# Performance work log

Measured on AMD Instinct MI355X. Metric: run time of the kernel, lower is better.

Reference implementation:

```python
import jax, jax.numpy as jnp
import numpy as np

N, L, S, D, K, H, G = 512, 1024, 3, 128, 4, 32, 64


def setup_inputs() -> dict:
    key = jax.random.key(0)
    ks = jax.random.split(key, 12)
    f = lambda i, shape, s=1.0: jax.random.normal(ks[i], shape, dtype=jnp.float32) * s
    return dict(
        scores=f(0, (N, 1, L, S)),
        veh_repr=f(1, (N, 1, D)),
        cust_repr=f(2, (N, L, D)),
        edge_emb=f(3, (N, 1, L, D)),
        expert_w1=f(4, (K, S, H), 0.3),
        expert_b1=jnp.zeros((K, H), jnp.float32),
        expert_w2=f(5, (K, H, 1), 0.3),
        expert_b2=jnp.zeros((K, 1), jnp.float32),
        sit_w1=f(6, (2 * D, G), 0.05),
        sit_b1=jnp.zeros((G,), jnp.float32),
        sit_w2=f(7, (G, K), 0.1),
        sit_b2=jnp.zeros((K,), jnp.float32),
        cand_w=f(8, (S, K), 0.3),
        cand_b=jnp.zeros((K,), jnp.float32),
        edge_w=f(9, (D, K), 0.05),
        gate_balance=jnp.zeros((), jnp.float32),
    )


def reference(scores, veh_repr, cust_repr, edge_emb,
              expert_w1, expert_b1, expert_w2, expert_b2,
              sit_w1, sit_b1, sit_w2, sit_b2,
              cand_w, cand_b, edge_w, gate_balance):
    # Inference mode: no gate noise, no dropout (identity at eval).
    # Situation gating: vehicle repr + graph context -> (N,1,K) logits
    graph_ctx = cust_repr.mean(axis=1, keepdims=True)              # (N,1,D)
    sit_in = jnp.concatenate([veh_repr, graph_ctx], axis=-1)       # (N,1,2D)
    hg = jax.nn.gelu(sit_in @ sit_w1 + sit_b1, approximate=False)  # (N,1,G)
    sit_logits = hg @ sit_w2 + sit_b2                              # (N,1,K)

    # Candidate-level gating from raw scores + edge embeddings
    cand_logits = scores @ cand_w + cand_b + edge_emb @ edge_w     # (N,1,L,K)

    alpha = jax.nn.sigmoid(gate_balance)
    gate_logits = alpha * sit_logits[:, :, None, :] + (1.0 - alpha) * cand_logits
    gate_w = jax.nn.softmax(gate_logits, axis=-1)                  # (N,1,L,K)

    # Per-expert tiny MLP over the S score channels
    h = jax.nn.gelu(jnp.einsum('nqls,ksh->nqlkh', scores, expert_w1) + expert_b1,
                    approximate=False)                             # (N,1,L,K,H)
    expert_out = jnp.einsum('nqlkh,kho->nqlko', h, expert_w2)[..., 0] + expert_b2[:, 0]

    fused = (gate_w * expert_out).sum(axis=-1)                     # (N,1,L)
    return fused
```

## Files before the change

### kernel.cpp

```cpp
#include <hip/hip_runtime.h>

#define NN 512
#define LL 1024
#define SS 3
#define DD 128
#define KK 4
#define HH 32
#define GG 64

#define DPP_XOR1 0xB1
#define DPP_XOR2 0x4E
#define DPP_ROR4 0x124
#define DPP_ROR8 0x128
#define SWZ16 0x401F

template <int CTRL>
__device__ __forceinline__ float dppf(float x) {
    return __int_as_float(__builtin_amdgcn_update_dpp(
        0, __float_as_int(x), CTRL, 0xF, 0xF, true));
}
__device__ __forceinline__ float swz16f(float x) {
    return __int_as_float(__builtin_amdgcn_ds_swizzle(__float_as_int(x), SWZ16));
}

__device__ __forceinline__ float fast_gelu(float x) {
    const float c0 = 0.7978845608028654f;
    const float c1 = 0.7978845608028654f * 0.044715f;
    float u = x * x;
    float y = x * fmaf(c1, u, c0);
    float e = __expf(2.0f * y);
    float r = __builtin_amdgcn_rcpf(e + 1.0f);
    float t = fmaf(-2.0f, r, 1.0f);
    return 0.5f * x * (1.0f + t);
}

__global__ __launch_bounds__(512, 4) void k_all(
    const float* __restrict__ scores, const float* __restrict__ veh,
    const float* __restrict__ cust, const float* __restrict__ edge,
    const float* __restrict__ ew1, const float* __restrict__ eb1,
    const float* __restrict__ ew2, const float* __restrict__ eb2,
    const float* __restrict__ sw1, const float* __restrict__ sb1,
    const float* __restrict__ sw2, const float* __restrict__ sb2,
    const float* __restrict__ cand_w, const float* __restrict__ cand_b,
    const float* __restrict__ edge_w, const float* __restrict__ gbp,
    float* __restrict__ out)
{
    __shared__ float4 red[512];
    __shared__ float sin_[2 * DD];
    __shared__ float hg[GG];
    __shared__ float slds[KK];
    __shared__ float4 sc4[(LL * SS) / 4];
    __shared__ float elds[LL * 8];

    const int n = blockIdx.x;
    const int t = threadIdx.x;
    const int lane = t & 63;
    const int r = lane & 31;

    const int ko = r & 3;
    const int jg = r >> 2;
    const bool kb0 = (r & 1) != 0;
    const bool kb1 = (r & 2) != 0;

    {
        const float4* sp4 = (const float4*)(scores + (size_t)n * LL * SS);
        sc4[t] = sp4[t];
        if (t < 256) sc4[512 + t] = sp4[512 + t];
    }

    const float4* ew4 = (const float4*)edge_w;
    const float4 wqa = ew4[4 * r + 0];
    const float4 wqb = ew4[4 * r + 1];
    const float4 wqc = ew4[4 * r + 2];
    const float4 wqd = ew4[4 * r + 3];
    const float cw0 = cand_w[0 * KK + ko];
    const float cw1 = cand_w[1 * KK + ko];
    const float cw2 = cand_w[2 * KK + ko];
    const float cb  = cand_b[ko];
    const float4* w1f = (const float4*)ew1;
    const float4 w1a = w1f[(ko * SS + 0) * (HH / 4) + jg];
    const float4 w1b = w1f[(ko * SS + 1) * (HH / 4) + jg];
    const float4 w1c = w1f[(ko * SS + 2) * (HH / 4) + jg];
    const float4 b1v = ((const float4*)eb1)[ko * (HH / 4) + jg];
    const float4 w2v = ((const float4*)ew2)[ko * (HH / 4) + jg];
    const float b2o8 = 0.125f * eb2[ko];
    const float gbv = gbp[0];
    const float alpha = 1.0f / (1.0f + __expf(-gbv));
    const float onema = 1.0f - alpha;
    const float cbase = onema * cb;

    __syncthreads();

    const int c = t & 31;
    const int rs = t >> 5;
    const float4* cp = (const float4*)(cust + (size_t)n * LL * DD);
    const int base_el = t >> 5;
    const float* sc_lds = (const float*)sc4;
    const float* ed_base = edge + (size_t)n * LL * DD;

    float4 a0 = make_float4(0.f, 0.f, 0.f, 0.f), a1 = a0, a2 = a0, a3 = a0;

    for (int i = 0; i < 16; ++i) {
        const int e0 = base_el + i * 64;

        float4 ev[4];
        #pragma unroll
        for (int u = 0; u < 4; ++u)
            ev[u] = *(const float4*)(ed_base + (size_t)(e0 + u * 16) * DD + r * 4);
        float4 v0 = cp[(rs + 16 * i      ) * 32 + c];
        float4 v1 = cp[(rs + 16 * i + 256) * 32 + c];
        float4 v2 = cp[(rs + 16 * i + 512) * 32 + c];
        float4 v3 = cp[(rs + 16 * i + 768) * 32 + c];

        float s0[4], s1[4], s2[4];
        #pragma unroll
        for (int u = 0; u < 4; ++u) {
            const int el = e0 + u * 16;
            s0[u] = sc_lds[el * 3 + 0];
            s1[u] = sc_lds[el * 3 + 1];
            s2[u] = sc_lds[el * 3 + 2];
        }

        float p0[4], p1[4], p2[4], p3[4];
        #pragma unroll
        for (int u = 0; u < 4; ++u) {
            p0[u] = fmaf(ev[u].x, wqa.x, fmaf(ev[u].y, wqb.x, fmaf(ev[u].z, wqc.x, ev[u].w * wqd.x)));
            p1[u] = fmaf(ev[u].x, wqa.y, fmaf(ev[u].y, wqb.y, fmaf(ev[u].z, wqc.y, ev[u].w * wqd.y)));
            p2[u] = fmaf(ev[u].x, wqa.z, fmaf(ev[u].y, wqb.z, fmaf(ev[u].z, wqc.z, ev[u].w * wqd.z)));
            p3[u] = fmaf(ev[u].x, wqa.w, fmaf(ev[u].y, wqb.w, fmaf(ev[u].z, wqc.w, ev[u].w * wqd.w)));
        }
        float P0[4], P2[4];
        #pragma unroll
        for (int u = 0; u < 4; ++u) {
            float g0 = kb0 ? p0[u] : p1[u];
            float g2 = kb0 ? p2[u] : p3[u];
            float k0 = kb0 ? p1[u] : p0[u];
            float k2 = kb0 ? p3[u] : p2[u];
            P0[u] = k0 + dppf<DPP_XOR1>(g0);
            P2[u] = k2 + dppf<DPP_XOR1>(g2);
        }
        float q[4];
        #pragma unroll
        for (int u = 0; u < 4; ++u) {
            float gv = kb1 ? P0[u] : P2[u];
            float kv = kb1 ? P2[u] : P0[u];
            q[u] = kv + dppf<DPP_XOR2>(gv);
        }
        #pragma unroll
        for (int u = 0; u < 4; ++u) q[u] += dppf<DPP_ROR4>(q[u]);
        #pragma unroll
        for (int u = 0; u < 4; ++u) q[u] += dppf<DPP_ROR8>(q[u]);
        #pragma unroll
        for (int u = 0; u < 4; ++u) q[u] += swz16f(q[u]);

        float exc[4];
        #pragma unroll
        for (int u = 0; u < 4; ++u) {
            float sdot = fmaf(s0[u], cw0, fmaf(s1[u], cw1, s2[u] * cw2));
            exc[u] = __expf(fmaf(onema, sdot + q[u], cbase));
        }

        float vq[4];
        #pragma unroll
        for (int u = 0; u < 4; ++u) {
            float z, h, acc;
            z = fmaf(s0[u], w1a.x, fmaf(s1[u], w1b.x, fmaf(s2[u], w1c.x, b1v.x))); h = fast_gelu(z); acc = h * w2v.x;
            z = fmaf(s0[u], w1a.y, fmaf(s1[u], w1b.y, fmaf(s2[u], w1c.y, b1v.y))); h = fast_gelu(z); acc = fmaf(h, w2v.y, acc);
            z = fmaf(s0[u], w1a.z, fmaf(s1[u], w1b.z, fmaf(s2[u], w1c.z, b1v.z))); h = fast_gelu(z); acc = fmaf(h, w2v.z, acc);
            z = fmaf(s0[u], w1a.w, fmaf(s1[u], w1b.w, fmaf(s2[u], w1c.w, b1v.w))); h = fast_gelu(z); acc = fmaf(h, w2v.w, acc);
            vq[u] = exc[u] * (acc + b2o8);
        }
        #pragma unroll
        for (int u = 0; u < 4; ++u) vq[u] += dppf<DPP_ROR4>(vq[u]);
        #pragma unroll
        for (int u = 0; u < 4; ++u) vq[u] += dppf<DPP_ROR8>(vq[u]);
        #pragma unroll
        for (int u = 0; u < 4; ++u) vq[u] += swz16f(vq[u]);

        if (r < 8) {
            #pragma unroll
            for (int u = 0; u < 4; ++u) {
                const int el = e0 + u * 16;
                elds[el * 8 + r] = (r < 4) ? vq[u] : exc[u];
            }
        }

        a0.x += v0.x; a0.y += v0.y; a0.z += v0.z; a0.w += v0.w;
        a1.x += v1.x; a1.y += v1.y; a1.z += v1.z; a1.w += v1.w;
        a2.x += v2.x; a2.y += v2.y; a2.z += v2.z; a2.w += v2.w;
        a3.x += v3.x; a3.y += v3.y; a3.z += v3.z; a3.w += v3.w;
    }

    a0.x += a1.x + a2.x + a3.x;
    a0.y += a1.y + a2.y + a3.y;
    a0.z += a1.z + a2.z + a3.z;
    a0.w += a1.w + a2.w + a3.w;
    red[t] = a0;
    __syncthreads();

    if (t < 32) {
        float4 s = red[t];
        #pragma unroll
        for (int i = 1; i < 16; i++) {
            float4 v = red[i * 32 + t];
            s.x += v.x; s.y += v.y; s.z += v.z; s.w += v.w;
        }
        const float inv = 1.0f / (float)LL;
        sin_[DD + 4 * t + 0] = s.x * inv;
        sin_[DD + 4 * t + 1] = s.y * inv;
        sin_[DD + 4 * t + 2] = s.z * inv;
        sin_[DD + 4 * t + 3] = s.w * inv;
        float4 vv = ((const float4*)(veh + (size_t)n * DD))[t];
        sin_[4 * t + 0] = vv.x; sin_[4 * t + 1] = vv.y;
        sin_[4 * t + 2] = vv.z; sin_[4 * t + 3] = vv.w;
    }
    __syncthreads();

    float* redf = (float*)red;
    if (t < 256) {
        const int g = t & 63;
        const int part = t >> 6;
        float a = 0.f;
        #pragma unroll 8
        for (int i = 0; i < 64; ++i) {
            const int row = part * 64 + i;
            a = fmaf(sin_[row], sw1[row * GG + g], a);
        }
        redf[t] = a;
    }
    __syncthreads();
    if (t < GG) {
        float a = sb1[t] + redf[t] + redf[t + 64] + redf[t + 128] + redf[t + 192];
        hg[t] = fast_gelu(a);
    }
    __syncthreads();
    if (t < KK) {
        float a = sb2[t];
        #pragma unroll
        for (int g = 0; g < GG; g++)
            a = fmaf(hg[g], sw2[g * KK + t], a);
        slds[t] = a;
    }
    __syncthreads();

    const float m0 = __expf(alpha * slds[0]);
    const float m1 = __expf(alpha * slds[1]);
    const float m2 = __expf(alpha * slds[2]);
    const float m3 = __expf(alpha * slds[3]);
    float* out_base = out + (size_t)n * LL;
    #pragma unroll
    for (int e = t; e < LL; e += 512) {
        const float4 V = *(const float4*)&elds[e * 8];
        const float4 E = *(const float4*)&elds[e * 8 + 4];
        float num = fmaf(m0, V.x, fmaf(m1, V.y, fmaf(m2, V.z, m3 * V.w)));
        float den = fmaf(m0, E.x, fmaf(m1, E.y, fmaf(m2, E.z, m3 * E.w)));
        out_base[e] = num * __builtin_amdgcn_rcpf(den);
    }
}

extern "C" void kernel_launch(void* const* d_in, const int* in_sizes, int n_in,
                              void* d_out, int out_size, void* d_ws, size_t ws_size,
                              hipStream_t stream)
{
    const float* scores = (const float*)d_in[0];
    const float* veh    = (const float*)d_in[1];
    const float* cust   = (const float*)d_in[2];
    const float* edge   = (const float*)d_in[3];
    const float* ew1    = (const float*)d_in[4];
    const float* eb1    = (const float*)d_in[5];
    const float* ew2    = (const float*)d_in[6];
    const float* eb2    = (const float*)d_in[7];
    const float* sw1    = (const float*)d_in[8];
    const float* sb1    = (const float*)d_in[9];
    const float* sw2    = (const float*)d_in[10];
    const float* sb2    = (const float*)d_in[11];
    const float* cw     = (const float*)d_in[12];
    const float* cb     = (const float*)d_in[13];
    const float* egw    = (const float*)d_in[14];
    const float* gb     = (const float*)d_in[15];
    float* out = (float*)d_out;

    hipLaunchKernelGGL(k_all, dim3(NN), dim3(512), 0, stream,
                       scores, veh, cust, edge, ew1, eb1, ew2, eb2,
                       sw1, sb1, sw2, sb2, cw, cb, egw, gb, out);
}
```

Baseline: 537.5 us.

## Software-pipeline edge embedding loads and alias score/reduction shared buffers

```diff
diff --git a/kernel.cpp b/kernel.cpp
--- a/kernel.cpp
+++ b/kernel.cpp
@@ -33,6 +33,94 @@
     float t = fmaf(-2.0f, r, 1.0f);
     return 0.5f * x * (1.0f + t);
 }
+
+#define BODY(I, EVC, EVN, PF)                                                   \
+  {                                                                             \
+    const int e0 = base_el + (I) * 64;                                          \
+                         \
+    float4 v0 = cp[(base_el + 16 * (I)      ) * 32 + r];                        \
+    float4 v1 = cp[(base_el + 16 * (I) + 256) * 32 + r];                        \
+    float4 v2 = cp[(base_el + 16 * (I) + 512) * 32 + r];                        \
+    float4 v3 = cp[(base_el + 16 * (I) + 768) * 32 + r];                        \
+    if (PF) {                                                                   \
+      _Pragma("unroll")                                                         \
+      for (int u = 0; u < 4; ++u)                                               \
+        EVN[u] = *(const float4*)(ed_base + (size_t)(e0 + 64 + u * 16) * DD + r * 4); \
+    }                                                                           \
+    float s0[4], s1[4], s2[4];                                                  \
+    _Pragma("unroll")                                                           \
+    for (int u = 0; u < 4; ++u) {                                               \
+      const int el = e0 + u * 16;                                               \
+      s0[u] = sc_lds[el * 3 + 0];                                               \
+      s1[u] = sc_lds[el * 3 + 1];                                               \
+      s2[u] = sc_lds[el * 3 + 2];                                               \
+    }                                                                           \
+    float p0[4], p1[4], p2[4], p3[4];                                           \
+    _Pragma("unroll")                                                           \
+    for (int u = 0; u < 4; ++u) {                                               \
+      p0[u] = fmaf(EVC[u].x, wqa.x, fmaf(EVC[u].y, wqb.x, fmaf(EVC[u].z, wqc.x, EVC[u].w * wqd.x))); \
+      p1[u] = fmaf(EVC[u].x, wqa.y, fmaf(EVC[u].y, wqb.y, fmaf(EVC[u].z, wqc.y, EVC[u].w * wqd.y))); \
+      p2[u] = fmaf(EVC[u].x, wqa.z, fmaf(EVC[u].y, wqb.z, fmaf(EVC[u].z, wqc.z, EVC[u].w * wqd.z))); \
+      p3[u] = fmaf(EVC[u].x, wqa.w, fmaf(EVC[u].y, wqb.w, fmaf(EVC[u].z, wqc.w, EVC[u].w * wqd.w))); \
+    }                                                                           \
+    float P0[4], P2[4];                                                         \
+    _Pragma("unroll")                                                           \
+    for (int u = 0; u < 4; ++u) {                                               \
+      float g0 = kb0 ? p0[u] : p1[u];                                           \
+      float g2 = kb0 ? p2[u] : p3[u];                                           \
+      float k0 = kb0 ? p1[u] : p0[u];                                           \
+      float k2 = kb0 ? p3[u] : p2[u];                                           \
+      P0[u] = k0 + dppf<DPP_XOR1>(g0);                                          \
+      P2[u] = k2 + dppf<DPP_XOR1>(g2);                                          \
+    }                                                                           \
+    float q[4];                                                                 \
+    _Pragma("unroll")                                                           \
+    for (int u = 0; u < 4; ++u) {                                               \
+      float gv = kb1 ? P0[u] : P2[u];                                           \
+      float kv = kb1 ? P2[u] : P0[u];                                           \
+      q[u] = kv + dppf<DPP_XOR2>(gv);                                           \
+    }                                                                           \
+    _Pragma("unroll")                                                           \
+    for (int u = 0; u < 4; ++u) q[u] += dppf<DPP_ROR4>(q[u]);                   \
+    _Pragma("unroll")                                                           \
+    for (int u = 0; u < 4; ++u) q[u] += dppf<DPP_ROR8>(q[u]);                   \
+    _Pragma("unroll")                                                           \
+    for (int u = 0; u < 4; ++u) q[u] += swz16f(q[u]);                           \
+    float exc[4];                                                               \
+    _Pragma("unroll")                                                           \
+    for (int u = 0; u < 4; ++u) {                                               \
+      float sdot = fmaf(s0[u], cw0, fmaf(s1[u], cw1, s2[u] * cw2));             \
+      exc[u] = __expf(fmaf(onema, sdot + q[u], cbase));                         \
+    }                                                                           \
+    float vq[4];                                                                \
+    _Pragma("unroll")                                                           \
+    for (int u = 0; u < 4; ++u) {                                               \
+      float z, h, acc;                                                          \
+      z = fmaf(s0[u], w1a.x, fmaf(s1[u], w1b.x, fmaf(s2[u], w1c.x, b1v.x))); h = fast_gelu(z); acc = h * w2v.x; \
+      z = fmaf(s0[u], w1a.y, fmaf(s1[u], w1b.y, fmaf(s2[u], w1c.y, b1v.y))); h = fast_gelu(z); acc = fmaf(h, w2v.y, acc); \
+      z = fmaf(s0[u], w1a.z, fmaf(s1[u], w1b.z, fmaf(s2[u], w1c.z, b1v.z))); h = fast_gelu(z); acc = fmaf(h, w2v.z, acc); \
+      z = fmaf(s0[u], w1a.w, fmaf(s1[u], w1b.w, fmaf(s2[u], w1c.w, b1v.w))); h = fast_gelu(z); acc = fmaf(h, w2v.w, acc); \
+      vq[u] = exc[u] * (acc + b2o8);                                            \
+    }                                                                           \
+    _Pragma("unroll")                                                           \
+    for (int u = 0; u < 4; ++u) vq[u] += dppf<DPP_ROR4>(vq[u]);                 \
+    _Pragma("unroll")                                                           \
+    for (int u = 0; u < 4; ++u) vq[u] += dppf<DPP_ROR8>(vq[u]);                 \
+    _Pragma("unroll")                                                           \
+    for (int u = 0; u < 4; ++u) vq[u] += swz16f(vq[u]);                         \
+    if (r < 8) {                                                                \
+      _Pragma("unroll")                                                         \
+      for (int u = 0; u < 4; ++u) {                                             \
+        const int el = e0 + u * 16;                                             \
+        elds[el * 8 + r] = (r < 4) ? vq[u] : exc[u];                            \
+      }                                                                         \
+    }                                                                           \
+             \
+    a0.x += (v0.x + v1.x) + (v2.x + v3.x);                                      \
+    a0.y += (v0.y + v1.y) + (v2.y + v3.y);                                      \
+    a0.z += (v0.z + v1.z) + (v2.z + v3.z);                                      \
+    a0.w += (v0.w + v1.w) + (v2.w + v3.w);                                      \
+  }
 
 __global__ __launch_bounds__(512, 4) void k_all(
     const float* __restrict__ scores, const float* __restrict__ veh,
@@ -45,17 +133,16 @@
     const float* __restrict__ edge_w, const float* __restrict__ gbp,
     float* __restrict__ out)
 {
-    __shared__ float4 red[512];
+    __shared__ float shbuf[3072];
     __shared__ float sin_[2 * DD];
     __shared__ float hg[GG];
     __shared__ float slds[KK];
-    __shared__ float4 sc4[(LL * SS) / 4];
     __shared__ float elds[LL * 8];
 
     const int n = blockIdx.x;
     const int t = threadIdx.x;
-    const int lane = t & 63;
-    const int r = lane & 31;
+    const int r = t & 31;
+    const int base_el = t >> 5;
 
     const int ko = r & 3;
     const int jg = r >> 2;
@@ -64,6 +151,7 @@
 
     {
         const float4* sp4 = (const float4*)(scores + (size_t)n * LL * SS);
+        float4* sc4 = (float4*)shbuf;
         sc4[t] = sp4[t];
         if (t < 256) sc4[512 + t] = sp4[512 + t];
     }
@@ -76,7 +164,6 @@
     const float cw0 = cand_w[0 * KK + ko];
     const float cw1 = cand_w[1 * KK + ko];
     const float cw2 = cand_w[2 * KK + ko];
-    const float cb  = cand_b[ko];
     const float4* w1f = (const float4*)ew1;
     const float4 w1a = w1f[(ko * SS + 0) * (HH / 4) + jg];
     const float4 w1b = w1f[(ko * SS + 1) * (HH / 4) + jg];
@@ -84,125 +171,40 @@
     const float4 b1v = ((const float4*)eb1)[ko * (HH / 4) + jg];
     const float4 w2v = ((const float4*)ew2)[ko * (HH / 4) + jg];
     const float b2o8 = 0.125f * eb2[ko];
-    const float gbv = gbp[0];
-    const float alpha = 1.0f / (1.0f + __expf(-gbv));
+    const float alpha = 1.0f / (1.0f + __expf(-gbp[0]));
     const float onema = 1.0f - alpha;
-    const float cbase = onema * cb;
-
-    __syncthreads();
-
-    const int c = t & 31;
-    const int rs = t >> 5;
+    const float cbase = onema * cand_b[ko];
+
+    __syncthreads();
+
+    const float* sc_lds = shbuf;
     const float4* cp = (const float4*)(cust + (size_t)n * LL * DD);
-    const int base_el = t >> 5;
-    const float* sc_lds = (const float*)sc4;
     const float* ed_base = edge + (size_t)n * LL * DD;
 
-    float4 a0 = make_float4(0.f, 0.f, 0.f, 0.f), a1 = a0, a2 = a0, a3 = a0;
-
-    for (int i = 0; i < 16; ++i) {
-        const int e0 = base_el + i * 64;
-
-        float4 ev[4];
-        #pragma unroll
-        for (int u = 0; u < 4; ++u)
-            ev[u] = *(const float4*)(ed_base + (size_t)(e0 + u * 16) * DD + r * 4);
-        float4 v0 = cp[(rs + 16 * i      ) * 32 + c];
-        float4 v1 = cp[(rs + 16 * i + 256) * 32 + c];
-        float4 v2 = cp[(rs + 16 * i + 512) * 32 + c];
-        float4 v3 = cp[(rs + 16 * i + 768) * 32 + c];
-
-        float s0[4], s1[4], s2[4];
-        #pragma unroll
-        for (int u = 0; u < 4; ++u) {
-            const int el = e0 + u * 16;
-            s0[u] = sc_lds[el * 3 + 0];
-            s1[u] = sc_lds[el * 3 + 1];
-            s2[u] = sc_lds[el * 3 + 2];
-        }
-
-        float p0[4], p1[4], p2[4], p3[4];
-        #pragma unroll
-        for (int u = 0; u < 4; ++u) {
-            p0[u] = fmaf(ev[u].x, wqa.x, fmaf(ev[u].y, wqb.x, fmaf(ev[u].z, wqc.x, ev[u].w * wqd.x)));
-            p1[u] = fmaf(ev[u].x, wqa.y, fmaf(ev[u].y, wqb.y, fmaf(ev[u].z, wqc.y, ev[u].w * wqd.y)));
-            p2[u] = fmaf(ev[u].x, wqa.z, fmaf(ev[u].y, wqb.z, fmaf(ev[u].z, wqc.z, ev[u].w * wqd.z)));
-            p3[u] = fmaf(ev[u].x, wqa.w, fmaf(ev[u].y, wqb.w, fmaf(ev[u].z, wqc.w, ev[u].w * wqd.w)));
-        }
-        float P0[4], P2[4];
-        #pragma unroll
-        for (int u = 0; u < 4; ++u) {
-            float g0 = kb0 ? p0[u] : p1[u];
-            float g2 = kb0 ? p2[u] : p3[u];
-            float k0 = kb0 ? p1[u] : p0[u];
-            float k2 = kb0 ? p3[u] : p2[u];
-            P0[u] = k0 + dppf<DPP_XOR1>(g0);
-            P2[u] = k2 + dppf<DPP_XOR1>(g2);
-        }
-        float q[4];
-        #pragma unroll
-        for (int u = 0; u < 4; ++u) {
-            float gv = kb1 ? P0[u] : P2[u];
-            float kv = kb1 ? P2[u] : P0[u];
-            q[u] = kv + dppf<DPP_XOR2>(gv);
-        }
-        #pragma unroll
-        for (int u = 0; u < 4; ++u) q[u] += dppf<DPP_ROR4>(q[u]);
-        #pragma unroll
-        for (int u = 0; u < 4; ++u) q[u] += dppf<DPP_ROR8>(q[u]);
-        #pragma unroll
-        for (int u = 0; u < 4; ++u) q[u] += swz16f(q[u]);
-
-        float exc[4];
-        #pragma unroll
-        for (int u = 0; u < 4; ++u) {
-            float sdot = fmaf(s0[u], cw0, fmaf(s1[u], cw1, s2[u] * cw2));
-            exc[u] = __expf(fmaf(onema, sdot + q[u], cbase));
-        }
-
-        float vq[4];
-        #pragma unroll
-        for (int u = 0; u < 4; ++u) {
-            float z, h, acc;
-            z = fmaf(s0[u], w1a.x, fmaf(s1[u], w1b.x, fmaf(s2[u], w1c.x, b1v.x))); h = fast_gelu(z); acc = h * w2v.x;
-            z = fmaf(s0[u], w1a.y, fmaf(s1[u], w1b.y, fmaf(s2[u], w1c.y, b1v.y))); h = fast_gelu(z); acc = fmaf(h, w2v.y, acc);
-            z = fmaf(s0[u], w1a.z, fmaf(s1[u], w1b.z, fmaf(s2[u], w1c.z, b1v.z))); h = fast_gelu(z); acc = fmaf(h, w2v.z, acc);
-            z = fmaf(s0[u], w1a.w, fmaf(s1[u], w1b.w, fmaf(s2[u], w1c.w, b1v.w))); h = fast_gelu(z); acc = fmaf(h, w2v.w, acc);
-            vq[u] = exc[u] * (acc + b2o8);
-        }
-        #pragma unroll
-        for (int u = 0; u < 4; ++u) vq[u] += dppf<DPP_ROR4>(vq[u]);
-        #pragma unroll
-        for (int u = 0; u < 4; ++u) vq[u] += dppf<DPP_ROR8>(vq[u]);
-        #pragma unroll
-        for (int u = 0; u < 4; ++u) vq[u] += swz16f(vq[u]);
-
-        if (r < 8) {
-            #pragma unroll
-            for (int u = 0; u < 4; ++u) {
-                const int el = e0 + u * 16;
-                elds[el * 8 + r] = (r < 4) ? vq[u] : exc[u];
-            }
-        }
-
-        a0.x += v0.x; a0.y += v0.y; a0.z += v0.z; a0.w += v0.w;
-        a1.x += v1.x; a1.y += v1.y; a1.z += v1.z; a1.w += v1.w;
-        a2.x += v2.x; a2.y += v2.y; a2.z += v2.z; a2.w += v2.w;
-        a3.x += v3.x; a3.y += v3.y; a3.z += v3.z; a3.w += v3.w;
-    }
-
-    a0.x += a1.x + a2.x + a3.x;
-    a0.y += a1.y + a2.y + a3.y;
-    a0.z += a1.z + a2.z + a3.z;
-    a0.w += a1.w + a2.w + a3.w;
-    red[t] = a0;
+    float4 ev_a[4], ev_b[4];
+    #pragma unroll
+    for (int u = 0; u < 4; ++u)
+        ev_a[u] = *(const float4*)(ed_base + (size_t)(base_el + u * 16) * DD + r * 4);
+
+    float4 a0 = make_float4(0.f, 0.f, 0.f, 0.f);
+
+    for (int ii = 0; ii < 14; ii += 2) {
+        BODY(ii,     ev_a, ev_b, 1)
+        BODY(ii + 1, ev_b, ev_a, 1)
+    }
+    BODY(14, ev_a, ev_b, 1)
+    BODY(15, ev_b, ev_a, 0)
+
+    __syncthreads();
+    float4* redv = (float4*)shbuf;
+    redv[t] = a0;
     __syncthreads();
 
     if (t < 32) {
-        float4 s = red[t];
+        float4 s = redv[t];
         #pragma unroll
         for (int i = 1; i < 16; i++) {
-            float4 v = red[i * 32 + t];
+            float4 v = redv[i * 32 + t];
             s.x += v.x; s.y += v.y; s.z += v.z; s.w += v.w;
         }
         const float inv = 1.0f / (float)LL;
@@ -216,7 +218,7 @@
     }
     __syncthreads();
 
-    float* redf = (float*)red;
+    float* redf = shbuf;
     if (t < 256) {
         const int g = t & 63;
         const int part = t >> 6;
```

New measurement: 559.4 us. 1.04x slower.
